# Kernel tuning notes

Measured on AMD Instinct MI355X. Metric: run time of the kernel, lower is better.

The kernel has to match this reference:

```python
import jax, jax.numpy as jnp
import numpy as np

N_SLICES, H, W = 64, 64, 64
VD, VH, VW = 64, 64, 64
K = 3            # PSF kernel size per axis
RES = 1.5        # res_s / res_r
GAP = 1.0        # through-plane slice spacing in recon voxels
N_ITER = 2       # CG iterations (init kwarg)


def _rotmat(ax, ay, az):
    cx, sx = np.cos(ax), np.sin(ax)
    cy, sy = np.cos(ay), np.sin(ay)
    cz, sz = np.cos(az), np.sin(az)
    Rx = np.array([[1, 0, 0], [0, cx, -sx], [0, sx, cx]])
    Ry = np.array([[cy, 0, sy], [0, 1, 0], [-sy, 0, cy]])
    Rz = np.array([[cz, -sz, 0], [sz, cz, 0], [0, 0, 1]])
    return Rz @ Ry @ Rx


def setup_inputs() -> dict:
    rng = np.random.default_rng(0)
    R = np.stack([_rotmat(*rng.normal(0.0, 0.05, 3)) for _ in range(N_SLICES)])
    t = np.zeros((N_SLICES, 3))
    t[:, :2] = rng.normal(0.0, 1.0, (N_SLICES, 2))
    t[:, 2] = (np.arange(N_SLICES) - (N_SLICES - 1) / 2) * GAP + rng.normal(0.0, 0.3, N_SLICES)
    transforms = jnp.asarray(np.concatenate([R, t[:, :, None]], -1), jnp.float32)  # (S,3,4)
    k1, k2 = jax.random.split(jax.random.key(0))
    slices = jax.random.uniform(k1, (N_SLICES, H, W), jnp.float32)
    volume = jax.random.uniform(k2, (VD, VH, VW), jnp.float32) * 0.1
    g = np.arange(K) - (K - 1) / 2
    gz, gy, gx = np.meshgrid(g, g, g, indexing='ij')
    psf = np.exp(-(gx ** 2 + gy ** 2) / (2 * 0.6 ** 2) - gz ** 2 / (2 * 1.0 ** 2))
    psf = jnp.asarray(psf / psf.sum(), jnp.float32)
    return {"transforms": transforms, "slices": slices, "volume": volume, "psf": psf}


def _positions(transforms):
    # PSF sample positions of every slice pixel, mapped into volume voxel coords (xyz).
    xs = (jnp.arange(W) - (W - 1) / 2) * RES
    ys = (jnp.arange(H) - (H - 1) / 2) * RES
    o = jnp.arange(K) - (K - 1) / 2
    oz, oy, ox = jnp.meshgrid(o, o, o, indexing='ij')
    off = jnp.stack([ox, oy, oz], -1).reshape(-1, 3)              # (K^3, 3)
    base = jnp.stack(jnp.broadcast_arrays(xs[None, :], ys[:, None], jnp.zeros((H, W))), -1)
    pts = base[None] + off[:, None, None, :]                      # (K^3, H, W, 3) slice frame
    R, tr = transforms[:, :, :3], transforms[:, :, 3]
    pos = jnp.einsum('sij,khwj->skhwi', R, pts) + tr[:, None, None, None, :]
    center = jnp.array([(VW - 1) / 2, (VH - 1) / 2, (VD - 1) / 2], jnp.float32)
    return pos + center                                           # (S, K^3, H, W, 3)


def _corner_iter(pos):
    # yields the 8 trilinear corners: (clipped int indices (z,y,x), weight with OOB zeroed)
    x, y, z = pos[..., 0], pos[..., 1], pos[..., 2]
    x0, y0, z0 = jnp.floor(x), jnp.floor(y), jnp.floor(z)
    fx, fy, fz = x - x0, y - y0, z - z0
    for dz in (0, 1):
        for dy in (0, 1):
            for dx in (0, 1):
                xi, yi, zi = x0 + dx, y0 + dy, z0 + dz
                w = (fx if dx else 1 - fx) * (fy if dy else 1 - fy) * (fz if dz else 1 - fz)
                valid = (xi >= 0) & (xi < VW) & (yi >= 0) & (yi < VH) & (zi >= 0) & (zi < VD)
                w = jnp.where(valid, w, 0.0)
                yield (jnp.clip(zi, 0, VD - 1).astype(jnp.int32),
                       jnp.clip(yi, 0, VH - 1).astype(jnp.int32),
                       jnp.clip(xi, 0, VW - 1).astype(jnp.int32)), w


def _A(vol, pos, psf_flat):
    # slice_acquisition: trilinear gather + PSF-weighted sum -> (S,H,W)
    acc = jnp.zeros(pos.shape[:-1], vol.dtype)
    for (zi, yi, xi), w in _corner_iter(pos):
        acc = acc + w * vol[zi, yi, xi]
    return jnp.einsum('k,skhw->shw', psf_flat, acc)


def _At(slc, pos, psf_flat):
    # slice_acquisition_adjoint: PSF-weighted trilinear scatter-add -> (VD,VH,VW)
    vals = psf_flat[None, :, None, None] * slc[:, None]           # (S,K^3,H,W)
    vol = jnp.zeros((VD, VH, VW), slc.dtype)
    for (zi, yi, xi), w in _corner_iter(pos):
        vol = vol.at[zi, yi, xi].add(w * vals)
    return vol


def _cg(Afun, b, x0, n_iter):
    x = x0
    r = b - Afun(x)
    p = r
    rr = jnp.vdot(r, r)
    for i in range(n_iter):
        Ap = Afun(p)
        alpha = rr / jnp.vdot(p, Ap)
        x = x + alpha * p
        if i == n_iter - 1:
            break
        r = r - alpha * Ap
        rr_new = jnp.vdot(r, r)
        p = r + (rr_new / rr) * p
        rr = rr_new
    return x


def reference(transforms, slices, volume, psf):
    pos = _positions(transforms)
    psf_flat = psf.reshape(-1)
    AtA = lambda v: _At(_A(v, pos, psf_flat), pos, psf_flat)
    b = _At(slices, pos, psf_flat)
    x = _cg(AtA, b, volume, N_ITER)
    return jax.nn.relu(x)
```

## Files before the change

### kernel.cpp

```cpp
#include <hip/hip_runtime.h>

#define NS 64
#define HH 64
#define WW 64
#define VD 64
#define VH 64
#define VW 64
#define NVOX (VD*VH*VW)
#define NPIX (NS*HH*WW)
#define RES 1.5f
#define NTAB (NS*27)
#define WIN 6
#define SPLIT 8
#define SLC_PER 8
#define COL_PAD 67

__global__ __launch_bounds__(256) void k_setup(const float* __restrict__ tr,
                                               const float* __restrict__ psf,
                                               float* __restrict__ tab) {
    int i = blockIdx.x * 256 + threadIdx.x;
    if (i >= NTAB) return;
    int s = i / 27, k = i % 27;
    const float* p = tr + s * 12;
    float R00 = p[0], R01 = p[1], R02 = p[2],  t0 = p[3];
    float R10 = p[4], R11 = p[5], R12 = p[6],  t1 = p[7];
    float R20 = p[8], R21 = p[9], R22 = p[10], t2 = p[11];
    float Ux = RES * R00, Uy = RES * R10, Uz = RES * R20;
    float Vx = RES * R01, Vy = RES * R11, Vz = RES * R21;
    float ox = (float)(k % 3 - 1), oy = (float)((k / 3) % 3 - 1), oz = (float)(k / 9 - 1);
    float Cx = t0 + 31.5f + R00 * ox + R01 * oy + R02 * oz - 31.5f * (Ux + Vx);
    float Cy = t1 + 31.5f + R10 * ox + R11 * oy + R12 * oz - 31.5f * (Uy + Vy);
    float Cz = t2 + 31.5f + R20 * ox + R21 * oy + R22 * oz - 31.5f * (Uz + Vz);
    float inv = 1.f / (Ux * Vy - Uy * Vx);
    float* e = tab + i * 16;
    e[0] = Vy * inv;  e[1] = -Vx * inv; e[2] = -Uy * inv; e[3] = Ux * inv;
    e[4] = Ux; e[5] = Uy; e[6] = Uz; e[7] = Vx;
    e[8] = Vy; e[9] = Vz; e[10] = Cx; e[11] = Cy;
    e[12] = Cz; e[13] = psf[k]; e[14] = 0.f; e[15] = 0.f;
}

__device__ __forceinline__ float trilin_gather_bf(const float* __restrict__ vol,
                                                  float px, float py, float pz) {
    float x0 = floorf(px), y0 = floorf(py), z0 = floorf(pz);
    float fx = px - x0, fy = py - y0, fz = pz - z0;
    int ix = (int)x0, iy = (int)y0, iz = (int)z0;

    float wx0 = ((unsigned)ix       < 64u) ? (1.f - fx) : 0.f;
    float wx1 = ((unsigned)(ix + 1) < 64u) ? fx         : 0.f;
    float wy0 = ((unsigned)iy       < 64u) ? (1.f - fy) : 0.f;
    float wy1 = ((unsigned)(iy + 1) < 64u) ? fy         : 0.f;
    float wz0 = ((unsigned)iz       < 64u) ? (1.f - fz) : 0.f;
    float wz1 = ((unsigned)(iz + 1) < 64u) ? fz         : 0.f;

    int xc0 = min(max(ix, 0), 63),     xc1 = min(max(ix + 1, 0), 63);
    int yc0 = min(max(iy, 0), 63) << 6,  yc1 = min(max(iy + 1, 0), 63) << 6;
    int zc0 = min(max(iz, 0), 63) << 12, zc1 = min(max(iz + 1, 0), 63) << 12;

    float v000 = vol[zc0 + yc0 + xc0], v001 = vol[zc0 + yc0 + xc1];
    float v010 = vol[zc0 + yc1 + xc0], v011 = vol[zc0 + yc1 + xc1];
    float v100 = vol[zc1 + yc0 + xc0], v101 = vol[zc1 + yc0 + xc1];
    float v110 = vol[zc1 + yc1 + xc0], v111 = vol[zc1 + yc1 + xc1];

    float w00 = wx0 * wy0, w01 = wx1 * wy0, w10 = wx0 * wy1, w11 = wx1 * wy1;
    float lo = fmaf(w00, v000, fmaf(w01, v001, fmaf(w10, v010, w11 * v011)));
    float hi = fmaf(w00, v100, fmaf(w01, v101, fmaf(w10, v110, w11 * v111)));
    return fmaf(wz0, lo, wz1 * hi);
}

__global__ __launch_bounds__(256) void k_a(const float* __restrict__ vin,
                                           float* __restrict__ g,
                                           const float* __restrict__ tr,
                                           const float* __restrict__ psf) {
    __shared__ float s_psf[27];
    if (threadIdx.x < 27) s_psf[threadIdx.x] = psf[threadIdx.x];
    __syncthreads();
    int gid = blockIdx.x * 256 + threadIdx.x;
    int pixel = gid >> 2, q = gid & 3;
    int s = pixel >> 12;
    int pix = pixel & 4095;
    int h = pix >> 6, w = pix & 63;
    const float* p = tr + s * 12;
    float R0 = p[0], R1 = p[1], R2 = p[2],  t0 = p[3];
    float R3 = p[4], R4 = p[5], R5 = p[6],  t1 = p[7];
    float R6 = p[8], R7 = p[9], R8 = p[10], t2 = p[11];
    float xs = ((float)w - 31.5f) * RES;
    float ys = ((float)h - 31.5f) * RES;
    float p0x = fmaf(R0, xs, fmaf(R1, ys, t0)) + 31.5f;
    float p0y = fmaf(R3, xs, fmaf(R4, ys, t1)) + 31.5f;
    float p0z = fmaf(R6, xs, fmaf(R7, ys, t2)) + 31.5f;
    float a = 0.f;
#pragma unroll
    for (int j = 0; j < 7; ++j) {
        int k = q + 4 * j;
        if (k < 27) {
            float ox = (float)(k % 3 - 1), oy = (float)((k / 3) % 3 - 1), oz = (float)(k / 9 - 1);
            float px = p0x + ox * R0 + oy * R1 + oz * R2;
            float py = p0y + ox * R3 + oy * R4 + oz * R5;
            float pz = p0z + ox * R6 + oy * R7 + oz * R8;
            a = fmaf(s_psf[k], trilin_gather_bf(vin, px, py, pz), a);
        }
    }
    a += __shfl_xor(a, 1);
    a += __shfl_xor(a, 2);
    if (q == 0) g[pixel] = a;
}

__device__ __forceinline__ void block_reduce_atomic(float v, float* dst) {
#pragma unroll
    for (int off = 32; off > 0; off >>= 1) v += __shfl_down(v, off, 64);
    __shared__ float s_red[4];
    int lane = threadIdx.x & 63, wid = threadIdx.x >> 6;
    if (lane == 0) s_red[wid] = v;
    __syncthreads();
    if (threadIdx.x == 0) atomicAdd(dst, s_red[0] + s_red[1] + s_red[2] + s_red[3]);
}

__global__ __launch_bounds__(512, 4) void k_atv(const float* __restrict__ g,
                                                float* __restrict__ part,
                                                const float* __restrict__ tab) {
    __shared__ float stab[SLC_PER * 27 * 16];
    __shared__ float cols[64][COL_PAD];

    int tid = threadIdx.x;
    int Yb = blockIdx.x >> 3;
    int split = blockIdx.x & 7;

    {
        const float4* src = (const float4*)(tab + split * SLC_PER * 27 * 16);
        float4* dst = (float4*)stab;
#pragma unroll
        for (int i = 0; i < 2; ++i) {
            int j = tid + i * 512;
            if (j < SLC_PER * 27 * 4) dst[j] = src[j];
        }
    }
    {
        float4* c4 = (float4*)&cols[0][0];
#pragma unroll
        for (int i = 0; i < 3; ++i) {
            int j = tid + i * 512;
            if (j < 1072) c4[j] = make_float4(0.f, 0.f, 0.f, 0.f);
        }
    }
    __syncthreads();

    int lane = tid & 63;
    int wave = tid >> 6;
    int s = split * SLC_PER + wave;
    float X = (float)lane, Y = (float)Yb;

    const float* tb = stab + wave * 27 * 16;
    int gbase = s << 12;

    const float* ec = tb + 13 * 16;
    float4 c0 = *(const float4*)(ec);
    float4 c1 = *(const float4*)(ec + 4);
    float4 c2 = *(const float4*)(ec + 8);
    float4 c3 = *(const float4*)(ec + 12);
    float rxc = X - c2.z, ryc = Y - c2.w;
    float wsc = c0.x * rxc + c0.y * ryc;
    float hsc = c0.z * rxc + c0.w * ryc;
    float pzc = fmaf(wsc, c1.z, fmaf(hsc, c2.y, c3.x));
    float basef = floorf(pzc) - 2.f;
    int   basei = (int)basef;

    float acc[WIN];
#pragma unroll
    for (int j = 0; j < WIN; ++j) acc[j] = 0.f;

    for (int k = 0; k < 27; ++k) {
        const float* e = tb + k * 16;
        float4 e0 = *(const float4*)(e);
        float4 e1 = *(const float4*)(e + 4);
        float4 e2 = *(const float4*)(e + 8);
        float4 e3 = *(const float4*)(e + 12);
        float Ux = e1.x, Uy = e1.y, Uz = e1.z, Vx = e1.w;
        float Vy = e2.x, Vz = e2.y;
        float Cxr = e2.z - X, Cyr = e2.w - Y;
        float psfk = e3.y;
        float ws = e0.x * (-Cxr) + e0.y * (-Cyr);
        float hs = e0.z * (-Cxr) + e0.w * (-Cyr);
        float w0f = floorf(ws), h0f = floorf(hs);
        int w0 = (int)w0f, h0 = (int)h0f;
#pragma unroll
        for (int dh = 0; dh < 2; ++dh) {
            float fh = h0f + (float)dh;
            int hi = h0 + dh;
            int hok = ((unsigned)hi < 64u) ? 1 : 0;
            int hc = min(max(hi, 0), 63);
            float tx = fmaf(fh, Vx, Cxr);
            float ty = fmaf(fh, Vy, Cyr);
            float tz = fmaf(fh, Vz, e3.x);
#pragma unroll
            for (int dw = 0; dw < 2; ++dw) {
                float fw = w0f + (float)dw;
                int wi = w0 + dw;
                int ok = ((unsigned)wi < 64u) ? hok : 0;
                int wc = min(max(wi, 0), 63);
                float ddx = fmaf(fw, Ux, tx);
                float ddy = fmaf(fw, Uy, ty);
                float wx = fmaxf(0.f, 1.f - fabsf(ddx));
                float wy = fmaxf(0.f, 1.f - fabsf(ddy));
                float gv = g[gbase + (hc << 6) + wc];
                float val = ok ? (wx * wy * psfk * gv) : 0.f;
                float prel = fmaf(fw, Uz, tz) - basef;
#pragma unroll
                for (int j = 0; j < WIN; ++j) {
                    float t = fmaxf(0.f, 1.f - fabsf(prel - (float)j));
                    acc[j] = fmaf(val, t, acc[j]);
                }
            }
        }
    }

#pragma unroll
    for (int j = 0; j < WIN; ++j) {
        int zj = basei + j;
        int okz = ((unsigned)zj < 64u);
        int zc = min(max(zj, 0), 63);
        atomicAdd(&cols[lane][zc], okz ? acc[j] : 0.f);
    }
    __syncthreads();

    float* pout = part + split * NVOX + (Yb << 6);
#pragma unroll
    for (int i = 0; i < 8; ++i) {
        int j = tid + i * 512;
        int z = j >> 6, x = j & 63;
        pout[(z << 12) + x] = cols[x][z];
    }
}


__device__ __forceinline__ float sum8(const float* __restrict__ part, int i) {
    float a = 0.f;
#pragma unroll
    for (int j = 0; j < SPLIT; ++j) a += part[j * NVOX + i];
    return a;
}

__global__ __launch_bounds__(256) void k_sum8(const float* __restrict__ part,
                                              float* __restrict__ vout) {
    int i = blockIdx.x * 256 + threadIdx.x;
    vout[i] = sum8(part, i);
}

__global__ __launch_bounds__(256) void k_residual8(const float* __restrict__ b,
                                                   const float* __restrict__ part,
                                                   float* __restrict__ r,
                                                   float* __restrict__ p,
                                                   float* __restrict__ scal) {
    int i = blockIdx.x * 256 + threadIdx.x;
    float rv = b[i] - sum8(part, i);
    r[i] = rv;
    p[i] = rv;
    block_reduce_atomic(rv * rv, &scal[0]);
}

__global__ __launch_bounds__(256) void k_dot_reduce8(const float* __restrict__ part,
                                                     const float* __restrict__ p,
                                                     float* __restrict__ Ap,
                                                     float* __restrict__ dst) {
    int i = blockIdx.x * 256 + threadIdx.x;
    float apv = sum8(part, i);
    Ap[i] = apv;
    block_reduce_atomic(p[i] * apv, dst);
}

__global__ __launch_bounds__(256) void k_dot8(const float* __restrict__ part,
                                              const float* __restrict__ p,
                                              float* __restrict__ dst) {
    int i = blockIdx.x * 256 + threadIdx.x;
    block_reduce_atomic(p[i] * sum8(part, i), dst);
}

__global__ __launch_bounds__(256) void k_update_xr(const float* __restrict__ x_in,
                                                   float* __restrict__ x_out,
                                                   float* __restrict__ r,
                                                   const float* __restrict__ p,
                                                   const float* __restrict__ Ap,
                                                   float* __restrict__ scal) {
    int i = blockIdx.x * 256 + threadIdx.x;
    float alpha = scal[0] / scal[1];
    x_out[i] = fmaf(alpha, p[i], x_in[i]);
    float rv = fmaf(-alpha, Ap[i], r[i]);
    r[i] = rv;
    block_reduce_atomic(rv * rv, &scal[2]);
}

__global__ __launch_bounds__(256) void k_update_p(float* __restrict__ p,
                                                  const float* __restrict__ r,
                                                  const float* __restrict__ scal) {
    int i = blockIdx.x * 256 + threadIdx.x;
    float beta = scal[2] / scal[0];
    p[i] = fmaf(beta, p[i], r[i]);
}

__global__ __launch_bounds__(256) void k_final(const float* __restrict__ x,
                                               const float* __restrict__ p,
                                               const float* __restrict__ scal,
                                               float* __restrict__ out) {
    int i = blockIdx.x * 256 + threadIdx.x;
    float alpha = scal[2] / scal[3];
    float v = fmaf(alpha, p[i], x[i]);
    out[i] = v > 0.f ? v : 0.f;
}

extern "C" void kernel_launch(void* const* d_in, const int* in_sizes, int n_in,
                              void* d_out, int out_size, void* d_ws, size_t ws_size,
                              hipStream_t stream) {
    const float* transforms = (const float*)d_in[0];
    const float* slices     = (const float*)d_in[1];
    const float* volume     = (const float*)d_in[2];
    const float* psf        = (const float*)d_in[3];
    float* out = (float*)d_out;

    float* tab    = (float*)d_ws;
    float* part   = tab    + NTAB * 16;
    float* vol_b  = part   + SPLIT * NVOX;
    float* vol_x  = vol_b  + NVOX;
    float* vol_r  = vol_x  + NVOX;
    float* vol_p  = vol_r  + NVOX;
    float* vol_Ap = vol_p  + NVOX;
    float* gbuf   = vol_Ap + NVOX;
    float* scal   = gbuf   + NPIX;

    const int ablk = 64 * SPLIT;
    const int fblk = NPIX * 4 / 256;
    const int vblk = NVOX / 256;

    hipMemsetAsync(scal, 0, 4 * sizeof(float), stream);

    k_setup<<<(NTAB + 255) / 256, 256, 0, stream>>>(transforms, psf, tab);

    k_atv<<<ablk, 512, 0, stream>>>(slices, part, tab);
    k_sum8<<<vblk, 256, 0, stream>>>(part, vol_b);

    k_a<<<fblk, 256, 0, stream>>>(volume, gbuf, transforms, psf);
    k_atv<<<ablk, 512, 0, stream>>>(gbuf, part, tab);
    k_residual8<<<vblk, 256, 0, stream>>>(vol_b, part, vol_r, vol_p, scal);

    k_a<<<fblk, 256, 0, stream>>>(vol_p, gbuf, transforms, psf);
    k_atv<<<ablk, 512, 0, stream>>>(gbuf, part, tab);
    k_dot_reduce8<<<vblk, 256, 0, stream>>>(part, vol_p, vol_Ap, &scal[1]);
    k_update_xr<<<vblk, 256, 0, stream>>>(volume, vol_x, vol_r, vol_p, vol_Ap, scal);
    k_update_p<<<vblk, 256, 0, stream>>>(vol_p, vol_r, scal);

    k_a<<<fblk, 256, 0, stream>>>(vol_p, gbuf, transforms, psf);
    k_atv<<<ablk, 512, 0, stream>>>(gbuf, part, tab);
    k_dot8<<<vblk, 256, 0, stream>>>(part, vol_p, &scal[3]);
    k_final<<<vblk, 256, 0, stream>>>(vol_x, vol_p, scal, out);
}
```

Before: 334.9 us.

## Fold initial residual into one adjoint and split atv blocks over x and taps

Computes the initial residual as A^T(slices - A x0) by subtracting slices inside the forward projection. This removes a separate adjoint pass and its reduction kernel. The adjoint kernel now processes half an x-row per block and splits the 27 PSF taps between two half-waves, doubling block count with smaller shared memory. Ap reuses the pixel buffer to save workspace. Floating-point summation order changes slightly.

```diff
diff --git a/kernel.cpp b/kernel.cpp
--- a/kernel.cpp
+++ b/kernel.cpp
@@ -12,7 +12,6 @@
 #define NTAB (NS*27)
 #define WIN 6
 #define SPLIT 8
-#define SLC_PER 8
 #define COL_PAD 67
 
 __global__ __launch_bounds__(256) void k_setup(const float* __restrict__ tr,
@@ -67,10 +66,12 @@
     return fmaf(wz0, lo, wz1 * hi);
 }
 
+template<bool SUB>
 __global__ __launch_bounds__(256) void k_a(const float* __restrict__ vin,
                                            float* __restrict__ g,
                                            const float* __restrict__ tr,
-                                           const float* __restrict__ psf) {
+                                           const float* __restrict__ psf,
+                                           const float* __restrict__ slc) {
     __shared__ float s_psf[27];
     if (threadIdx.x < 27) s_psf[threadIdx.x] = psf[threadIdx.x];
     __syncthreads();
@@ -102,7 +103,7 @@
     }
     a += __shfl_xor(a, 1);
     a += __shfl_xor(a, 2);
-    if (q == 0) g[pixel] = a;
+    if (q == 0) g[pixel] = SUB ? (slc[pixel] - a) : a;
 }
 
 __device__ __forceinline__ void block_reduce_atomic(float v, float* dst) {
@@ -115,41 +116,44 @@
     if (threadIdx.x == 0) atomicAdd(dst, s_red[0] + s_red[1] + s_red[2] + s_red[3]);
 }
 
-__global__ __launch_bounds__(512, 4) void k_atv(const float* __restrict__ g,
+__global__ __launch_bounds__(512, 8) void k_atv(const float* __restrict__ g,
                                                 float* __restrict__ part,
                                                 const float* __restrict__ tab) {
-    __shared__ float stab[SLC_PER * 27 * 16];
-    __shared__ float cols[64][COL_PAD];
+    __shared__ float stab[8 * 27 * 16];
+    __shared__ float cols[32][COL_PAD];
 
     int tid = threadIdx.x;
-    int Yb = blockIdx.x >> 3;
+    int Yb    = blockIdx.x >> 4;
+    int xhalf = (blockIdx.x >> 3) & 1;
     int split = blockIdx.x & 7;
 
     {
-        const float4* src = (const float4*)(tab + split * SLC_PER * 27 * 16);
+        const float4* src = (const float4*)(tab + split * 8 * 27 * 16);
         float4* dst = (float4*)stab;
 #pragma unroll
         for (int i = 0; i < 2; ++i) {
             int j = tid + i * 512;
-            if (j < SLC_PER * 27 * 4) dst[j] = src[j];
+            if (j < 864) dst[j] = src[j];
         }
     }
     {
         float4* c4 = (float4*)&cols[0][0];
 #pragma unroll
-        for (int i = 0; i < 3; ++i) {
+        for (int i = 0; i < 2; ++i) {
             int j = tid + i * 512;
-            if (j < 1072) c4[j] = make_float4(0.f, 0.f, 0.f, 0.f);
+            if (j < 536) c4[j] = make_float4(0.f, 0.f, 0.f, 0.f);
         }
     }
     __syncthreads();
 
-    int lane = tid & 63;
-    int wave = tid >> 6;
-    int s = split * SLC_PER + wave;
-    float X = (float)lane, Y = (float)Yb;
-
-    const float* tb = stab + wave * 27 * 16;
+    int xl   = tid & 31;
+    int half = (tid >> 5) & 1;
+    int sg   = tid >> 6;
+    int s    = split * 8 + sg;
+    float X = (float)(xhalf * 32 + xl);
+    float Y = (float)Yb;
+
+    const float* tb = stab + sg * 27 * 16;
     int gbase = s << 12;
 
     const float* ec = tb + 13 * 16;
@@ -168,7 +172,9 @@
 #pragma unroll
     for (int j = 0; j < WIN; ++j) acc[j] = 0.f;
 
-    for (int k = 0; k < 27; ++k) {
+    int kbeg = half * 14;
+    int kend = kbeg + 14 - half;
+    for (int k = kbeg; k < kend; ++k) {
         const float* e = tb + k * 16;
         float4 e0 = *(const float4*)(e);
         float4 e1 = *(const float4*)(e + 4);
@@ -218,15 +224,15 @@
         int zj = basei + j;
         int okz = ((unsigned)zj < 64u);
         int zc = min(max(zj, 0), 63);
-        atomicAdd(&cols[lane][zc], okz ? acc[j] : 0.f);
+        atomicAdd(&cols[xl][zc], okz ? acc[j] : 0.f);
     }
     __syncthreads();
 
-    float* pout = part + split * NVOX + (Yb << 6);
-#pragma unroll
-    for (int i = 0; i < 8; ++i) {
+    float* pout = part + split * NVOX + (Yb << 6) + xhalf * 32;
+#pragma unroll
+    for (int i = 0; i < 4; ++i) {
         int j = tid + i * 512;
-        int z = j >> 6, x = j & 63;
+        int z = j >> 5, x = j & 31;
         pout[(z << 12) + x] = cols[x][z];
     }
 }
@@ -239,19 +245,12 @@
     return a;
 }
 
-__global__ __launch_bounds__(256) void k_sum8(const float* __restrict__ part,
-                                              float* __restrict__ vout) {
-    int i = blockIdx.x * 256 + threadIdx.x;
-    vout[i] = sum8(part, i);
-}
-
-__global__ __launch_bounds__(256) void k_residual8(const float* __restrict__ b,
-                                                   const float* __restrict__ part,
+__global__ __launch_bounds__(256) void k_residual8(const float* __restrict__ part,
                                                    float* __restrict__ r,
                                                    float* __restrict__ p,
                                                    float* __restrict__ scal) {
     int i = blockIdx.x * 256 + threadIdx.x;
-    float rv = b[i] - sum8(part, i);
+    float rv = sum8(part, i);
     r[i] = rv;
     p[i] = rv;
     block_reduce_atomic(rv * rv, &scal[0]);
@@ -317,15 +316,14 @@
 
     float* tab    = (float*)d_ws;
     float* part   = tab    + NTAB * 16;
-    float* vol_b  = part   + SPLIT * NVOX;
-    float* vol_x  = vol_b  + NVOX;
+    float* vol_x  = part   + SPLIT * NVOX;
     float* vol_r  = vol_x  + NVOX;
     float* vol_p  = vol_r  + NVOX;
-    float* vol_Ap = vol_p  + NVOX;
-    float* gbuf   = vol_Ap + NVOX;
+    float* gbuf   = vol_p  + NVOX;
     float* scal   = gbuf   + NPIX;
-
-    const int ablk = 64 * SPLIT;
+    float* Ap     = gbuf;
+
+    const int ablk = 64 * 2 * SPLIT;
     const int fblk = NPIX * 4 / 256;
     const int vblk = NVOX / 256;
 
@@ -333,20 +331,17 @@
 
     k_setup<<<(NTAB + 255) / 256, 256, 0, stream>>>(transforms, psf, tab);
 
-    k_atv<<<ablk, 512, 0, stream>>>(slices, part, tab);
-    k_sum8<<<vblk, 256, 0, stream>>>(part, vol_b);
-
-    k_a<<<fblk, 256, 0, stream>>>(volume, gbuf, transforms, psf);
+    k_a<true><<<fblk, 256, 0, stream>>>(volume, gbuf, transforms, psf, slices);
     k_atv<<<ablk, 512, 0, stream>>>(gbuf, part, tab);
-    k_residual8<<<vblk, 256, 0, stream>>>(vol_b, part, vol_r, vol_p, scal);
-
-    k_a<<<fblk, 256, 0, stream>>>(vol_p, gbuf, transforms, psf);
+    k_residual8<<<vblk, 256, 0, stream>>>(part, vol_r, vol_p, scal);
+
+    k_a<false><<<fblk, 256, 0, stream>>>(vol_p, gbuf, transforms, psf, nullptr);
     k_atv<<<ablk, 512, 0, stream>>>(gbuf, part, tab);
-    k_dot_reduce8<<<vblk, 256, 0, stream>>>(part, vol_p, vol_Ap, &scal[1]);
-    k_update_xr<<<vblk, 256, 0, stream>>>(volume, vol_x, vol_r, vol_p, vol_Ap, scal);
+    k_dot_reduce8<<<vblk, 256, 0, stream>>>(part, vol_p, Ap, &scal[1]);
+    k_update_xr<<<vblk, 256, 0, stream>>>(volume, vol_x, vol_r, vol_p, Ap, scal);
     k_update_p<<<vblk, 256, 0, stream>>>(vol_p, vol_r, scal);
 
-    k_a<<<fblk, 256, 0, stream>>>(vol_p, gbuf, transforms, psf);
+    k_a<false><<<fblk, 256, 0, stream>>>(vol_p, gbuf, transforms, psf, nullptr);
     k_atv<<<ablk, 512, 0, stream>>>(gbuf, part, tab);
     k_dot8<<<vblk, 256, 0, stream>>>(part, vol_p, &scal[3]);
     k_final<<<vblk, 256, 0, stream>>>(vol_x, vol_p, scal, out);
```

Result: faster. 298.0 us (-11.0%).
